# Optimization experiments

Hardware: AMD Instinct MI355X
Metric: run time of the kernel (lower is better)

## Reference

```python
import jax, jax.numpy as jnp
import numpy as np

N = 4096            # net_input_dim (number of nodes)
S0, S1, S2 = 256, 128, 64   # net_shape
TAU = 0.5
THRESH = 0.9        # threshold[2]
REC, MI, ME, MA, NEGC = 1.0, 0.1, 0.1, 0.1, 1.0
K_CLIQUE, K_NEIGH = 8, 16


def setup_inputs() -> dict:
    key = jax.random.key(0)
    ks = jax.random.split(key, 12)
    return {
        "A": jax.random.normal(ks[0], (N, N), dtype=jnp.float32),
        "U0": jax.random.uniform(ks[1], (N, S0), dtype=jnp.float32),
        "U1": jax.random.uniform(ks[2], (S0, S1), dtype=jnp.float32),
        "U2": jax.random.uniform(ks[3], (S1, S2), dtype=jnp.float32),
        "V2": jax.random.uniform(ks[4], (S2, N), dtype=jnp.float32),
        "fc1_w": jax.random.normal(ks[5], (S1, S2), dtype=jnp.float32) * 0.05,
        "fc1_b": jnp.zeros((S1,), dtype=jnp.float32),
        "fc2_w": jax.random.normal(ks[6], (S0, S1), dtype=jnp.float32) * 0.05,
        "fc2_b": jnp.zeros((S0,), dtype=jnp.float32),
        "sim_mat": jax.random.uniform(ks[7], (N, N), dtype=jnp.float32),
        "clique_idx": jax.random.randint(ks[8], (N, K_CLIQUE), 0, N),
        "neighbor_idx": jax.random.randint(ks[9], (N, K_NEIGH), 0, N),
    }


def _l2norm_rows(z):
    # F.normalize(z) with default dim=1, eps=1e-12
    n = jnp.linalg.norm(z, axis=1, keepdims=True)
    return z / jnp.maximum(n, 1e-12)


def _mask_from_idx(idx):
    # per-row scatter: mask[i, idx[i, :]] = 1
    rows = jnp.arange(N)[:, None]
    return jnp.zeros((N, N), dtype=jnp.float32).at[rows, idx].set(1.0)


def _contrastive(refl_sim, mask):
    pos_sum = (refl_sim * mask).sum(axis=1)
    neg_sum = (refl_sim * (1.0 - mask)).sum(axis=1)
    cl = pos_sum / (pos_sum + neg_sum)
    cl = jnp.where(cl == 0, 1.0, cl)
    return -jnp.log(cl).sum() / N


def reference(A, U0, U1, U2, V2, fc1_w, fc1_b, fc2_w, fc2_b, sim_mat,
              clique_idx, neighbor_idx):
    # forward(): V1 = V['net2']
    V1 = V2  # [S2, N]

    # loss1: squared Frobenius norm of A - U0 U1 U2 V2 (eye(N) @ U0 == U0)
    P1 = ((U0 @ U1) @ U2) @ V2  # [N, N]
    loss1 = jnp.sum(jnp.square(A - P1))

    # projection1(V1): elu(fc1(V1.T)) -> fc2
    h = jax.nn.elu(V1.T @ fc1_w.T + fc1_b)   # [N, S1]
    h = h @ fc2_w.T + fc2_b                  # [N, S0]

    # exp(cosine sim / tau) -- identical matrix is rebuilt in each loss_*,
    # math is the same so compute it once
    hn = _l2norm_rows(h)
    refl_sim = jnp.exp((hn @ hn.T) / TAU)    # [N, N]

    loss2 = _contrastive(refl_sim, _mask_from_idx(clique_idx))     # loss_micro
    loss3 = _contrastive(refl_sim, _mask_from_idx(neighbor_idx))   # loss_meso
    loss4 = _contrastive(refl_sim, (sim_mat > THRESH).astype(jnp.float32))  # loss_sim

    # loss5: nonnegativity penalty on all factors
    loss5 = jnp.float32(0.0)
    for X in (U0, U1, U2, V2):
        loss5 = loss5 + jnp.sum(jnp.square(jnp.minimum(X, 0.0)))

    total = REC * loss1 + MI * loss2 + ME * loss3 + MA * loss4 + NEGC * loss5
    return jnp.stack([total, loss1, loss2, loss3, loss4, loss5])
```

## Files before the change

### kernel.cpp

```cpp
#include <hip/hip_runtime.h>
#include <math.h>
#include <stdint.h>

#define N 4096
#define S0 256
#define S1 128
#define S2 64
#define LDK 72

typedef __bf16 bf16;
typedef __attribute__((ext_vector_type(8))) __bf16 bf16x8;
typedef __attribute__((ext_vector_type(4))) __bf16 bf16x4;
typedef __attribute__((ext_vector_type(4))) float f32x4;
typedef unsigned long long u64;


__global__ __launch_bounds__(128) void k_prep(const float* __restrict__ U0,
                                              const float* __restrict__ U1,
                                              const float* __restrict__ U2,
                                              const float* __restrict__ V2,
                                              const float* __restrict__ fc1_w,
                                              const float* __restrict__ fc1_b,
                                              const float* __restrict__ fc2_w,
                                              const float* __restrict__ fc2_b,
                                              float* __restrict__ W,
                                              float* __restrict__ Wt,
                                              bf16* __restrict__ V2b,
                                              bf16* __restrict__ hnb,
                                              float* __restrict__ accz,
                                              float* __restrict__ ls5,
                                              const float* __restrict__ sim,
                                              u64* __restrict__ mask) {
    __shared__ __align__(16) char pb[12416];
    int bid = blockIdx.x;
    int tid = threadIdx.x;
    int lane = tid & 63, wv = tid >> 6;

    if (bid < 512) {
        float (*u0s)[S0]      = (float(*)[S0])pb;
        float (*ts)[S1 + 4]   = (float(*)[S1 + 4])(pb + 8192);
        int i0 = bid * 8;
        float ns = 0.f;

        for (int t = tid; t < 8 * S0; t += 128) {
            float x = U0[(i0 + (t >> 8)) * S0 + (t & 255)];
            u0s[t >> 8][t & 255] = x;
            if (x < 0.f) ns += x * x;
        }
        __syncthreads();
        {
            int j = tid;
            float acc[8] = {};
#pragma unroll 8
            for (int k = 0; k < S0; ++k) {
                float u1 = U1[k * S1 + j];
#pragma unroll
                for (int r = 0; r < 8; ++r) acc[r] += u0s[r][k] * u1;
            }
            for (int r = 0; r < 8; ++r) ts[r][j] = acc[r];
        }
        __syncthreads();
        {
            int j = tid & 63, h = tid >> 6;
            float acc2[4] = {};
#pragma unroll 8
            for (int k = 0; k < S1; ++k) {
                float u2 = U2[k * S2 + j];
#pragma unroll
                for (int r = 0; r < 4; ++r) acc2[r] += ts[h * 4 + r][k] * u2;
            }
            for (int r = 0; r < 4; ++r) {
                int i = i0 + h * 4 + r;
                W[i * S2 + j] = acc2[r];
                Wt[(size_t)j * N + i] = acc2[r];
            }
        }
        {
            for (int off = 32; off; off >>= 1) ns += __shfl_down(ns, off, 64);
            __syncthreads();
            float* nsr = (float*)pb;
            if (lane == 0) nsr[wv] = ns;
            __syncthreads();
            if (tid == 0) ls5[bid] = nsr[0] + nsr[1];
        }
    } else if (bid < 1024) {
        float (*vs)[S2]       = (float(*)[S2])pb;
        float (*hs)[S1 + 4]   = (float(*)[S1 + 4])(pb + 2048);
        float (*red)[8]       = (float(*)[8])(pb + 6272);
        float *norms          = (float*)(pb + 6336);
        int i0 = (bid - 512) * 8;

        for (int t = tid; t < 8 * S2; t += 128) {
            int r = t & 7, k = t >> 3;
            vs[r][k] = V2[k * N + i0 + r];
        }
        __syncthreads();
        {
            int j = tid;
            float b = fc1_b[j];
            float acc[8];
#pragma unroll
            for (int r = 0; r < 8; ++r) acc[r] = b;
#pragma unroll 4
            for (int kk = 0; kk < S2; kk += 4) {
                float4 w4 = *(const float4*)(fc1_w + j * S2 + kk);
#pragma unroll
                for (int r = 0; r < 8; ++r) {
                    float4 v4 = *(const float4*)(&vs[r][kk]);
                    acc[r] += v4.x * w4.x + v4.y * w4.y + v4.z * w4.z + v4.w * w4.w;
                }
            }
            for (int r = 0; r < 8; ++r) {
                float x = acc[r];
                hs[r][j] = x > 0.f ? x : (expf(x) - 1.f);
            }
        }
        __syncthreads();
        {
            int j = tid;
            float b0 = fc2_b[j], b1 = fc2_b[j + 128];
            float a0[8], a1[8];
#pragma unroll
            for (int r = 0; r < 8; ++r) { a0[r] = b0; a1[r] = b1; }
#pragma unroll 4
            for (int kk = 0; kk < S1; kk += 4) {
                float4 w0 = *(const float4*)(fc2_w + j * S1 + kk);
                float4 w1 = *(const float4*)(fc2_w + (j + 128) * S1 + kk);
#pragma unroll
                for (int r = 0; r < 8; ++r) {
                    float4 h4 = *(const float4*)(&hs[r][kk]);
                    a0[r] += h4.x * w0.x + h4.y * w0.y + h4.z * w0.z + h4.w * w0.w;
                    a1[r] += h4.x * w1.x + h4.y * w1.y + h4.z * w1.z + h4.w * w1.w;
                }
            }
#pragma unroll
            for (int r = 0; r < 8; ++r) {
                float v = a0[r] * a0[r] + a1[r] * a1[r];
                for (int off = 32; off; off >>= 1) v += __shfl_down(v, off, 64);
                if (lane == 0) red[wv][r] = v;
            }
            __syncthreads();
            if (tid < 8) norms[tid] = fmaxf(sqrtf(red[0][tid] + red[1][tid]), 1e-12f);
            __syncthreads();
            for (int r = 0; r < 8; ++r) {
                float inv = 1.f / norms[r];
                hnb[(i0 + r) * S0 + j] = (bf16)(a0[r] * inv);
                hnb[(i0 + r) * S0 + j + 128] = (bf16)(a1[r] * inv);
            }
        }
    } else if (bid < 1088) {
        int nb = bid - 1024;
        float ns = 0.f;
#pragma unroll
        for (int it = 0; it < 8; ++it) {
            int fi = nb * 1024 + it * 128 + tid;
            float4 x = *(const float4*)(V2 + (size_t)fi * 4);
            bf16x4 v = {(bf16)x.x, (bf16)x.y, (bf16)x.z, (bf16)x.w};
            *(bf16x4*)(V2b + (size_t)fi * 4) = v;
            if (x.x < 0.f) ns += x.x * x.x;
            if (x.y < 0.f) ns += x.y * x.y;
            if (x.z < 0.f) ns += x.z * x.z;
            if (x.w < 0.f) ns += x.w * x.w;
        }
        for (int off = 32; off; off >>= 1) ns += __shfl_down(ns, off, 64);
        float* nsr = (float*)pb;
        if (lane == 0) nsr[wv] = ns;
        __syncthreads();
        if (tid == 0) ls5[512 + nb] = nsr[0] + nsr[1];
    } else if (bid == 1088) {
        float ns = 0.f;
        for (int t = tid; t < (S0 * S1 + S1 * S2) / 4; t += 128) {
            float4 x = (t < S0 * S1 / 4) ? ((const float4*)U1)[t]
                                         : ((const float4*)U2)[t - S0 * S1 / 4];
            if (x.x < 0.f) ns += x.x * x.x;
            if (x.y < 0.f) ns += x.y * x.y;
            if (x.z < 0.f) ns += x.z * x.z;
            if (x.w < 0.f) ns += x.w * x.w;
        }
        for (int t = tid; t < 4 * N + 8; t += 128) accz[t] = 0.f;
        for (int off = 32; off; off >>= 1) ns += __shfl_down(ns, off, 64);
        float* nsr = (float*)pb;
        if (lane == 0) nsr[wv] = ns;
        __syncthreads();
        if (tid == 0) ls5[576] = nsr[0] + nsr[1];
    } else {
        int row = (bid - 1089) * 2 + wv;
        const float* base = sim + (size_t)row * N + lane * 4;
#pragma unroll
        for (int half = 0; half < 2; ++half) {
            float4 x[8];
#pragma unroll
            for (int it = 0; it < 8; ++it)
                x[it] = *(const float4*)(base + (half * 8 + it) * 256);
#pragma unroll
            for (int it = 0; it < 8; ++it) {
                u64 b0 = __ballot(x[it].x > 0.9f);
                u64 b1 = __ballot(x[it].y > 0.9f);
                u64 b2 = __ballot(x[it].z > 0.9f);
                u64 b3 = __ballot(x[it].w > 0.9f);
                if (lane < 4) {
                    u64 v = (lane == 0) ? b0 : (lane == 1) ? b1 : (lane == 2) ? b2 : b3;
                    mask[(size_t)row * 64 + (half * 8 + it) * 4 + lane] = v;
                }
            }
        }
    }
}


__global__ __launch_bounds__(256) void k_work(const bf16* __restrict__ hnb,
                                              const u64* __restrict__ mask,
                                              float* __restrict__ rowsum,
                                              float* __restrict__ pos4,
                                              const int* __restrict__ cIdx,
                                              const int* __restrict__ nIdx,
                                              float* __restrict__ pos2,
                                              float* __restrict__ pos3,
                                              const float* __restrict__ V2,
                                              const float* __restrict__ A,
                                              const bf16* __restrict__ V2b,
                                              const float* __restrict__ W,
                                              const float* __restrict__ Wt,
                                              double* __restrict__ lacc,
                                              double* __restrict__ pairsum) {
    __shared__ __align__(16) bf16 As[128 * LDK];
    __shared__ __align__(16) bf16 Bs[128 * LDK];
    __shared__ float rs_l[128], ps_l[128];
    int bid = blockIdx.x;
    int tid = threadIdx.x;
    int lane = tid & 63, w = tid >> 6;

    if (bid >= 1024 && bid < 1408) {
        int g = (bid - 1024) * 256 + tid;
        if (g >= N * 24) return;
        int i = g / 24, s = g % 24;
        const int* idx;
        int kk;
        float* dst;
        if (s < 8) { idx = cIdx + i * 8; kk = s; dst = pos2; }
        else       { idx = nIdx + i * 16; kk = s - 8; dst = pos3; }
        int t = idx[kk];
        for (int k = 0; k < kk; ++k)
            if (idx[k] == t) return;
        const bf16* a = hnb + i * S0;
        const bf16* b = hnb + t * S0;
        float dsum = 0.f;
        for (int k = 0; k < S0; k += 8) {
            bf16x8 av = *(const bf16x8*)(a + k);
            bf16x8 bv = *(const bf16x8*)(b + k);
#pragma unroll
            for (int u = 0; u < 8; ++u) dsum += (float)av[u] * (float)bv[u];
        }
        atomicAdd(dst + i, __expf(2.f * dsum));
        return;
    }

    if (bid >= 1408 && bid < 1920) {
        float* reds = (float*)As;
        float* redc = reds + 4;
        int b = bid - 1408;
        int split = b >> 5, rb = b & 31;
        int i0 = rb * 128, k0 = split * 256;
        int q = lane >> 4, l15 = lane & 15;

        f32x4 zero = {0.f, 0.f, 0.f, 0.f};
        f32x4 acc[2][4];
#pragma unroll
        for (int a = 0; a < 2; ++a)
#pragma unroll
            for (int c = 0; c < 4; ++c) acc[a][c] = zero;
        float a2 = 0.f;

        const float* arow = A + (size_t)(i0 + w * 32 + l15) * N + q * 8;
        for (int ch = 0; ch < 8; ++ch) {
            int jb = k0 + ch * 32;
            float4 xa0 = *(const float4*)(arow + jb);
            float4 xa1 = *(const float4*)(arow + jb + 4);
            float4 xb0 = *(const float4*)(arow + (size_t)16 * N + jb);
            float4 xb1 = *(const float4*)(arow + (size_t)16 * N + jb + 4);
            bf16x8 bfr[4];
#pragma unroll
            for (int tb = 0; tb < 4; ++tb)
                bfr[tb] = *(const bf16x8*)(V2b + (size_t)(tb * 16 + l15) * N + jb + q * 8);
            a2 += xa0.x * xa0.x + xa0.y * xa0.y + xa0.z * xa0.z + xa0.w * xa0.w;
            a2 += xa1.x * xa1.x + xa1.y * xa1.y + xa1.z * xa1.z + xa1.w * xa1.w;
            a2 += xb0.x * xb0.x + xb0.y * xb0.y + xb0.z * xb0.z + xb0.w * xb0.w;
            a2 += xb1.x * xb1.x + xb1.y * xb1.y + xb1.z * xb1.z + xb1.w * xb1.w;
            bf16x8 af0 = {(bf16)xa0.x, (bf16)xa0.y, (bf16)xa0.z, (bf16)xa0.w,
                          (bf16)xa1.x, (bf16)xa1.y, (bf16)xa1.z, (bf16)xa1.w};
            bf16x8 af1 = {(bf16)xb0.x, (bf16)xb0.y, (bf16)xb0.z, (bf16)xb0.w,
                          (bf16)xb1.x, (bf16)xb1.y, (bf16)xb1.z, (bf16)xb1.w};
#pragma unroll
            for (int tb = 0; tb < 4; ++tb) {
                acc[0][tb] = __builtin_amdgcn_mfma_f32_16x16x32_bf16(af0, bfr[tb], acc[0][tb], 0, 0, 0);
                acc[1][tb] = __builtin_amdgcn_mfma_f32_16x16x32_bf16(af1, bfr[tb], acc[1][tb], 0, 0, 0);
            }
        }
        float cr = 0.f;
#pragma unroll
        for (int ta = 0; ta < 2; ++ta)
#pragma unroll
            for (int v = 0; v < 4; ++v) {
                int i = i0 + w * 32 + ta * 16 + q * 4 + v;
                const float* wrow = W + (size_t)i * S2 + l15;
#pragma unroll
                for (int tb = 0; tb < 4; ++tb)
                    cr += wrow[tb * 16] * acc[ta][tb][v];
            }
        for (int off = 32; off; off >>= 1) {
            cr += __shfl_down(cr, off, 64);
            a2 += __shfl_down(a2, off, 64);
        }
        if (lane == 0) { reds[w] = a2; redc[w] = cr; }
        __syncthreads();
        if (tid == 0) {
            atomicAdd(lacc + 0, (double)(reds[0] + reds[1] + reds[2] + reds[3]));
            atomicAdd(lacc + 2, (double)(redc[0] + redc[1] + redc[2] + redc[3]));
        }
        return;
    }

    if (bid >= 1920) {
        double* gred = (double*)As;
        int p = (bid - 1920) * 4 + w;
        int kk = (int)((129.0 - sqrt(16641.0 - 8.0 * (double)p)) * 0.5);
        while ((kk + 1) * (129 - (kk + 1)) / 2 <= p) ++kk;
        while (kk * (129 - kk) / 2 > p) --kk;
        int ll = kk + (p - kk * (129 - kk) / 2);
        const float* wk = Wt + (size_t)kk * N;
        const float* wl = Wt + (size_t)ll * N;
        const float* vk = V2 + (size_t)kk * N;
        const float* vl = V2 + (size_t)ll * N;
        float s1 = 0.f, s2 = 0.f;
        for (int it = 0; it < 16; ++it) {
            int j = it * 256 + lane * 4;
            float4 a1 = *(const float4*)(wk + j);
            float4 b1 = *(const float4*)(wl + j);
            float4 a2v = *(const float4*)(vk + j);
            float4 b2v = *(const float4*)(vl + j);
            s1 += a1.x * b1.x + a1.y * b1.y + a1.z * b1.z + a1.w * b1.w;
            s2 += a2v.x * b2v.x + a2v.y * b2v.y + a2v.z * b2v.z + a2v.w * b2v.w;
        }
        for (int off = 32; off; off >>= 1) {
            s1 += __shfl_down(s1, off, 64);
            s2 += __shfl_down(s2, off, 64);
        }
        if (lane == 0) gred[w] = (double)s1 * (double)s2 * ((kk == ll) ? 1.0 : 2.0);
        __syncthreads();
        if (tid == 0)
            pairsum[bid - 1920] = gred[0] + gred[1] + gred[2] + gred[3];
        return;
    }

    int i0 = (bid >> 5) * 128, j0 = (bid & 31) * 128;
    int wm = (w >> 1) * 64, wn = (w & 1) * 64;
    if (tid < 128) { rs_l[tid] = 0.f; ps_l[tid] = 0.f; }

    f32x4 zero = {0.f, 0.f, 0.f, 0.f};
    f32x4 d[4][4];
#pragma unroll
    for (int a = 0; a < 4; ++a)
#pragma unroll
        for (int b = 0; b < 4; ++b) d[a][b] = zero;

    int q = lane >> 4, l15 = lane & 15;
    for (int k0 = 0; k0 < S0; k0 += 64) {
        __syncthreads();
#pragma unroll
        for (int t = 0; t < 4; ++t) {
            int idx = tid + 256 * t;
            int r = idx >> 3, c = idx & 7;
            uint4 va = *(const uint4*)(hnb + (i0 + r) * S0 + k0 + c * 8);
            uint4 vb = *(const uint4*)(hnb + (j0 + r) * S0 + k0 + c * 8);
            *(uint4*)(As + r * LDK + c * 8) = va;
            *(uint4*)(Bs + r * LDK + c * 8) = vb;
        }
        __syncthreads();
#pragma unroll
        for (int kk = 0; kk < 64; kk += 32) {
            bf16x8 af[4], bfr[4];
#pragma unroll
            for (int ta = 0; ta < 4; ++ta)
                af[ta] = *(const bf16x8*)(As + (wm + ta * 16 + l15) * LDK + kk + q * 8);
#pragma unroll
            for (int tb = 0; tb < 4; ++tb)
                bfr[tb] = *(const bf16x8*)(Bs + (wn + tb * 16 + l15) * LDK + kk + q * 8);
#pragma unroll
            for (int ta = 0; ta < 4; ++ta)
#pragma unroll
                for (int tb = 0; tb < 4; ++tb)
                    d[ta][tb] = __builtin_amdgcn_mfma_f32_16x16x32_bf16(af[ta], bfr[tb], d[ta][tb], 0, 0, 0);
        }
    }
    __syncthreads();
    u64* mwords = (u64*)As;
    int stripe = j0 >> 8, half = (j0 >> 7) & 1;
    for (int t = tid; t < 512; t += 256) {
        int li = t >> 2, u = t & 3;
        mwords[t] = mask[(size_t)(i0 + li) * 64 + stripe * 4 + u];
    }
    __syncthreads();
    int bitbase = half * 32 + (wn >> 2) + (l15 >> 2);
    int uoff = l15 & 3;
#pragma unroll
    for (int ta = 0; ta < 4; ++ta)
#pragma unroll
        for (int v = 0; v < 4; ++v) {
            int li = wm + ta * 16 + q * 4 + v;
            u64 word = mwords[li * 4 + uoff];
            float rs = 0.f, ps = 0.f;
#pragma unroll
            for (int tb = 0; tb < 4; ++tb) {
                float s = __expf(2.f * d[ta][tb][v]);
                rs += s;
                ps += ((word >> (bitbase + tb * 4)) & 1ULL) ? s : 0.f;
            }
#pragma unroll
            for (int m = 1; m < 16; m <<= 1) {
                rs += __shfl_xor(rs, m, 16);
                ps += __shfl_xor(ps, m, 16);
            }
            if (l15 == 0) {
                atomicAdd(&rs_l[li], rs);
                atomicAdd(&ps_l[li], ps);
            }
        }
    __syncthreads();
    if (tid < 128) {
        atomicAdd(&rowsum[i0 + tid], rs_l[tid]);
        atomicAdd(&pos4[i0 + tid], ps_l[tid]);
    }
}


__global__ __launch_bounds__(256) void k_final(const float* __restrict__ rowsum,
                                               const float* __restrict__ pos2,
                                               const float* __restrict__ pos3,
                                               const float* __restrict__ pos4,
                                               const double* __restrict__ lacc,
                                               const double* __restrict__ pairsum,
                                               const float* __restrict__ ls5,
                                               float* __restrict__ out) {
    __shared__ double red[5][4];
    int tid = threadIdx.x;
    double l2 = 0, l3 = 0, l4 = 0, sp = 0, l5 = 0;
    for (int i = tid; i < N; i += 256) {
        double rs = (double)rowsum[i];
        float p2 = pos2[i], p3 = pos3[i], p4 = pos4[i];
        if (p2 > 0.f) l2 -= log((double)p2 / rs);
        if (p3 > 0.f) l3 -= log((double)p3 / rs);
        if (p4 > 0.f) l4 -= log((double)p4 / rs);
    }
    for (int i = tid; i < 520; i += 256) sp += pairsum[i];
    for (int i = tid; i < 577; i += 256) l5 += (double)ls5[i];
    int lane = tid & 63, wave = tid >> 6;
    for (int off = 32; off; off >>= 1) {
        l2 += __shfl_down(l2, off, 64);
        l3 += __shfl_down(l3, off, 64);
        l4 += __shfl_down(l4, off, 64);
        sp += __shfl_down(sp, off, 64);
        l5 += __shfl_down(l5, off, 64);
    }
    if (lane == 0) { red[0][wave] = l2; red[1][wave] = l3; red[2][wave] = l4; red[3][wave] = sp; red[4][wave] = l5; }
    __syncthreads();
    if (tid == 0) {
        double L2 = 0, L3 = 0, L4 = 0, SP = 0, L5 = 0;
        for (int w = 0; w < 4; ++w) {
            L2 += red[0][w]; L3 += red[1][w]; L4 += red[2][w]; SP += red[3][w]; L5 += red[4][w];
        }
        L2 /= N; L3 /= N; L4 /= N;
        double L1 = lacc[0] - 2.0 * lacc[2] + SP;
        double total = L1 + 0.1 * (L2 + L3 + L4) + L5;
        out[0] = (float)total;
        out[1] = (float)L1;
        out[2] = (float)L2;
        out[3] = (float)L3;
        out[4] = (float)L4;
        out[5] = (float)L5;
    }
}

extern "C" void kernel_launch(void* const* d_in, const int* in_sizes, int n_in,
                              void* d_out, int out_size, void* d_ws, size_t ws_size,
                              hipStream_t stream) {
    const float* A     = (const float*)d_in[0];
    const float* U0    = (const float*)d_in[1];
    const float* U1    = (const float*)d_in[2];
    const float* U2    = (const float*)d_in[3];
    const float* V2    = (const float*)d_in[4];
    const float* fc1_w = (const float*)d_in[5];
    const float* fc1_b = (const float*)d_in[6];
    const float* fc2_w = (const float*)d_in[7];
    const float* fc2_b = (const float*)d_in[8];
    const float* sim   = (const float*)d_in[9];
    const int* cIdx    = (const int*)d_in[10];
    const int* nIdx    = (const int*)d_in[11];

    float* ws = (float*)d_ws;
    float* rowsum = ws;
    float* pos2 = ws + N;
    float* pos3 = ws + 2 * N;
    float* pos4 = ws + 3 * N;
    double* lacc = (double*)(ws + 4 * N);
    double* pairsum = lacc + 4;
    u64* mask = (u64*)(pairsum + 1024);
    bf16* hnb = (bf16*)(mask + (size_t)N * 64);
    float* W  = (float*)(hnb + (size_t)N * S0);
    float* Wt = W + (size_t)N * S2;
    bf16* V2b = (bf16*)(Wt + (size_t)S2 * N);
    float* ls5 = (float*)(V2b + (size_t)S2 * N);

    k_prep<<<3137, 128, 0, stream>>>(U0, U1, U2, V2, fc1_w, fc1_b, fc2_w, fc2_b,
                                     W, Wt, V2b, hnb, ws, ls5, sim, mask);
    k_work<<<2440, 256, 0, stream>>>(hnb, mask, rowsum, pos4, cIdx, nIdx,
                                     pos2, pos3, V2, A, V2b, W, Wt,
                                     lacc, pairsum);
    k_final<<<1, 256, 0, stream>>>(rowsum, pos2, pos3, pos4, lacc, pairsum, ls5,
                                   (float*)d_out);
}
```

Baseline: 262.4 us.

## Exploit symmetry of cosine-similarity matrix to compute only upper-triangular tiles

The Gram matrix hn·hnᵀ is symmetric, so the similarity GEMM now covers only the 528 upper-triangular 128×128 tiles instead of all 1024. Each off-diagonal tile also produces column sums and masked column sums, using the transposed mask words, and adds them into the rows of the mirrored block. This roughly halves the MFMA and exp work of the dominant GEMM phase. In exchange it adds extra mask loads, shuffles and shared and global atomics per tile, and it reads the sim_mat-derived mask transposed, which is valid only because the mask lookup is per (row, col) bit.

New measurement: 255.3 us. -2.7%, faster.

```diff
diff --git a/kernel.cpp b/kernel.cpp
--- a/kernel.cpp
+++ b/kernel.cpp
@@ -226,12 +226,13 @@
     __shared__ __align__(16) bf16 As[128 * LDK];
     __shared__ __align__(16) bf16 Bs[128 * LDK];
     __shared__ float rs_l[128], ps_l[128];
+    __shared__ float rs_c[128], ps_c[128];
     int bid = blockIdx.x;
     int tid = threadIdx.x;
     int lane = tid & 63, w = tid >> 6;
 
-    if (bid >= 1024 && bid < 1408) {
-        int g = (bid - 1024) * 256 + tid;
+    if (bid >= 528 && bid < 912) {
+        int g = (bid - 528) * 256 + tid;
         if (g >= N * 24) return;
         int i = g / 24, s = g % 24;
         const int* idx;
@@ -255,10 +256,10 @@
         return;
     }
 
-    if (bid >= 1408 && bid < 1920) {
+    if (bid >= 912 && bid < 1424) {
         float* reds = (float*)As;
         float* redc = reds + 4;
-        int b = bid - 1408;
+        int b = bid - 912;
         int split = b >> 5, rb = b & 31;
         int i0 = rb * 128, k0 = split * 256;
         int q = lane >> 4, l15 = lane & 15;
@@ -320,9 +321,9 @@
         return;
     }
 
-    if (bid >= 1920) {
+    if (bid >= 1424) {
         double* gred = (double*)As;
-        int p = (bid - 1920) * 4 + w;
+        int p = (bid - 1424) * 4 + w;
         int kk = (int)((129.0 - sqrt(16641.0 - 8.0 * (double)p)) * 0.5);
         while ((kk + 1) * (129 - (kk + 1)) / 2 <= p) ++kk;
         while (kk * (129 - kk) / 2 > p) --kk;
@@ -348,13 +349,21 @@
         if (lane == 0) gred[w] = (double)s1 * (double)s2 * ((kk == ll) ? 1.0 : 2.0);
         __syncthreads();
         if (tid == 0)
-            pairsum[bid - 1920] = gred[0] + gred[1] + gred[2] + gred[3];
+            pairsum[bid - 1424] = gred[0] + gred[1] + gred[2] + gred[3];
         return;
     }
 
-    int i0 = (bid >> 5) * 128, j0 = (bid & 31) * 128;
+    int p = bid;
+    int ti = (int)((65.0 - sqrt(4225.0 - 8.0 * (double)p)) * 0.5);
+    while ((ti + 1) * (65 - (ti + 1)) / 2 <= p) ++ti;
+    while (ti * (65 - ti) / 2 > p) --ti;
+    int tj = ti + (p - ti * (65 - ti) / 2);
+    int i0 = ti * 128, j0 = tj * 128;
+    bool diag = (ti == tj);
+
     int wm = (w >> 1) * 64, wn = (w & 1) * 64;
-    if (tid < 128) { rs_l[tid] = 0.f; ps_l[tid] = 0.f; }
+    int q = lane >> 4, l15 = lane & 15;
+    if (tid < 128) { rs_l[tid] = 0.f; ps_l[tid] = 0.f; rs_c[tid] = 0.f; ps_c[tid] = 0.f; }
 
     f32x4 zero = {0.f, 0.f, 0.f, 0.f};
     f32x4 d[4][4];
@@ -363,7 +372,6 @@
 #pragma unroll
         for (int b = 0; b < 4; ++b) d[a][b] = zero;
 
-    int q = lane >> 4, l15 = lane & 15;
     for (int k0 = 0; k0 < S0; k0 += 64) {
         __syncthreads();
 #pragma unroll
@@ -393,42 +401,72 @@
         }
     }
     __syncthreads();
-    u64* mwords = (u64*)As;
-    int stripe = j0 >> 8, half = (j0 >> 7) & 1;
+    u64* mwords  = (u64*)As;
+    u64* mwordsT = (u64*)Bs;
+    int stripe  = j0 >> 8, half  = (j0 >> 7) & 1;
+    int stripei = i0 >> 8, halfi = (i0 >> 7) & 1;
     for (int t = tid; t < 512; t += 256) {
         int li = t >> 2, u = t & 3;
         mwords[t] = mask[(size_t)(i0 + li) * 64 + stripe * 4 + u];
+        if (!diag)
+            mwordsT[t] = mask[(size_t)(j0 + li) * 64 + stripei * 4 + u];
     }
     __syncthreads();
     int bitbase = half * 32 + (wn >> 2) + (l15 >> 2);
     int uoff = l15 & 3;
+    float cs[4] = {0.f, 0.f, 0.f, 0.f};
+    float csp[4] = {0.f, 0.f, 0.f, 0.f};
 #pragma unroll
     for (int ta = 0; ta < 4; ++ta)
 #pragma unroll
         for (int v = 0; v < 4; ++v) {
             int li = wm + ta * 16 + q * 4 + v;
             u64 word = mwords[li * 4 + uoff];
+            int bitT = halfi * 32 + (wm >> 2) + ta * 4 + q;
             float rs = 0.f, ps = 0.f;
 #pragma unroll
             for (int tb = 0; tb < 4; ++tb) {
                 float s = __expf(2.f * d[ta][tb][v]);
                 rs += s;
                 ps += ((word >> (bitbase + tb * 4)) & 1ULL) ? s : 0.f;
+                cs[tb] += s;
+                if (!diag) {
+                    u64 wt = mwordsT[(wn + tb * 16 + l15) * 4 + v];
+                    csp[tb] += ((wt >> bitT) & 1ULL) ? s : 0.f;
+                }
             }
 #pragma unroll
             for (int m = 1; m < 16; m <<= 1) {
-                rs += __shfl_xor(rs, m, 16);
-                ps += __shfl_xor(ps, m, 16);
+                rs += __shfl_xor(rs, m, 64);
+                ps += __shfl_xor(ps, m, 64);
             }
             if (l15 == 0) {
                 atomicAdd(&rs_l[li], rs);
                 atomicAdd(&ps_l[li], ps);
             }
         }
+    if (!diag) {
+#pragma unroll
+        for (int tb = 0; tb < 4; ++tb) {
+            float c1 = cs[tb], c2 = csp[tb];
+            c1 += __shfl_xor(c1, 16, 64);
+            c1 += __shfl_xor(c1, 32, 64);
+            c2 += __shfl_xor(c2, 16, 64);
+            c2 += __shfl_xor(c2, 32, 64);
+            if (lane < 16) {
+                atomicAdd(&rs_c[wn + tb * 16 + l15], c1);
+                atomicAdd(&ps_c[wn + tb * 16 + l15], c2);
+            }
+        }
+    }
     __syncthreads();
     if (tid < 128) {
         atomicAdd(&rowsum[i0 + tid], rs_l[tid]);
         atomicAdd(&pos4[i0 + tid], ps_l[tid]);
+        if (!diag) {
+            atomicAdd(&rowsum[j0 + tid], rs_c[tid]);
+            atomicAdd(&pos4[j0 + tid], ps_c[tid]);
+        }
     }
 }
 
@@ -512,7 +550,7 @@
 
     k_prep<<<3137, 128, 0, stream>>>(U0, U1, U2, V2, fc1_w, fc1_b, fc2_w, fc2_b,
                                      W, Wt, V2b, hnb, ws, ls5, sim, mask);
-    k_work<<<2440, 256, 0, stream>>>(hnb, mask, rowsum, pos4, cIdx, nIdx,
+    k_work<<<1944, 256, 0, stream>>>(hnb, mask, rowsum, pos4, cIdx, nIdx,
                                      pos2, pos3, V2, A, V2b, W, Wt,
                                      lacc, pairsum);
     k_final<<<1, 256, 0, stream>>>(rowsum, pos2, pos3, pos4, lacc, pairsum, ls5,
```
